# Kernel tuning notes

Hardware: AMD Instinct MI355X
Metric: run time of the kernel (lower is better)

Reference implementation:

```python
import jax, jax.numpy as jnp
import numpy as np

D_DIM = 1024
K_DIM = 16
B, L = 4, 2048

def setup_inputs() -> dict:
    key = jax.random.key(0)
    kx, ky, kz, kw, kb = jax.random.split(key, 5)
    x = jax.random.normal(kx, (B, L, D_DIM), dtype=jnp.float32)
    y = jax.random.normal(ky, (B, L, D_DIM), dtype=jnp.float32)
    z = jax.random.normal(kz, (B, L, D_DIM), dtype=jnp.float32)
    bound = 1.0 / np.sqrt(3 * D_DIM)  # torch Linear init scale
    W = jax.random.uniform(kw, (K_DIM * D_DIM, 3 * D_DIM), dtype=jnp.float32, minval=-bound, maxval=bound)
    b = jax.random.uniform(kb, (K_DIM * D_DIM,), dtype=jnp.float32, minval=-bound, maxval=bound)
    return {"x": x, "y": y, "z": z, "W": W, "b": b}

def reference(x, y, z, W, b):
    Bsz, Lsz, D = x.shape
    inp = jnp.concatenate([x, y, z], axis=-1)                 # (B, L, 3D)
    kernel = jnp.einsum('blc,fc->blf', inp, W) + b            # (B, L, k*D)
    kernel = kernel.reshape(Bsz, Lsz, D, K_DIM)               # (B, L, D, k)
    # einsum 'bldk,bld->bld' == sum over k, then elementwise multiply
    return kernel.sum(axis=-1) * (x * y)
```

## Files before the change

kernel.cpp:

```cpp
#include <hip/hip_runtime.h>

#define M_ROWS 8192
#define N_DIM  1024
#define K3     3072
#define KD     16
#define NKT    48
#define BM     256
#define BN     128
#define BK     64
#define LDS_A  (BM * BK)
#define LDS_B  (BN * BK)
#define LDS_TILE (LDS_A + LDS_B)

typedef __bf16 bf16x8 __attribute__((ext_vector_type(8)));
typedef float  f32x4  __attribute__((ext_vector_type(4)));

__device__ __forceinline__ unsigned short f2bf(float f) {
  return __builtin_bit_cast(unsigned short, (__bf16)f);
}
__device__ __forceinline__ float bf2f(unsigned short u) {
  return __builtin_bit_cast(float, (unsigned int)u << 16);
}
__device__ __forceinline__ ushort4 pack4(f32x4 f) {
  ushort4 o; o.x = f2bf(f.x); o.y = f2bf(f.y); o.z = f2bf(f.z); o.w = f2bf(f.w);
  return o;
}
__device__ __forceinline__ f32x4 ntld4(const f32x4* p) {
  return __builtin_nontemporal_load(p);
}

__device__ __forceinline__ void async16(const void* g, void* l) {
  __builtin_amdgcn_global_load_lds(
      (const __attribute__((address_space(1))) unsigned int*)g,
      (__attribute__((address_space(3))) unsigned int*)l, 16, 0, 0);
}

__global__ __launch_bounds__(256) void wsum_kernel(
    const f32x4* __restrict__ W4, const float* __restrict__ b,
    ushort4* __restrict__ Wsum4, float* __restrict__ bsum)
{
  int bid = blockIdx.x;
  int tid = threadIdx.x;
  if (bid < 3072) {
    int g  = bid * 256 + tid;
    int d  = g / 768;
    int cq = g - d * 768;
    const f32x4* wrow = W4 + (size_t)d * (KD * K3 / 4);
    f32x4 s = ntld4(&wrow[cq]);
    #pragma unroll
    for (int k = 1; k < KD; ++k)
      s += ntld4(&wrow[(size_t)k * (K3 / 4) + cq]);
    Wsum4[g] = pack4(s);
  } else {
    int d = (bid - 3072) * 256 + tid;
    if (d < N_DIM) {
      float s = 0.f;
      #pragma unroll
      for (int k = 0; k < KD; ++k) s += b[d * KD + k];
      bsum[d] = s;
    }
  }
}

__global__ __launch_bounds__(256) void convert_kernel(
    const f32x4* __restrict__ x, const f32x4* __restrict__ y, const f32x4* __restrict__ z,
    ushort4* __restrict__ Ib4, ushort4* __restrict__ P4)
{
  int bid = blockIdx.x;
  int tid = threadIdx.x;
  int i = bid * 256 + tid;
  f32x4 fx = ntld4(&x[i]), fy = ntld4(&y[i]), fz = ntld4(&z[i]);
  size_t rb = (size_t)bid * 768;
  Ib4[rb + tid]       = pack4(fx);
  Ib4[rb + 256 + tid] = pack4(fy);
  Ib4[rb + 512 + tid] = pack4(fz);
  P4[i] = pack4(fx * fy);
}

__global__ __launch_bounds__(512, 2) void gemm_ep_kernel(
    const unsigned short* __restrict__ Ib, const unsigned short* __restrict__ Wsum,
    const float* __restrict__ bsum, const unsigned short* __restrict__ P,
    float* __restrict__ out)
{
  extern __shared__ unsigned short lds[];

  int bid = blockIdx.x;
  int swz = (bid & 7) * 32 + (bid >> 3);
  int mt = swz >> 3;
  int nt = swz & 7;
  int m0 = mt * BM, n0 = nt * BN;

  int tid  = threadIdx.x;
  int lane = tid & 63;
  int wid  = tid >> 6;
  int wr = wid >> 1, wc = wid & 1;
  int fr = lane & 15;
  int hi = lane >> 4;

  int row0 = tid >> 3;
  int ch0  = tid & 7;
  int dofs = tid * 16;
  int sc   = (ch0 ^ (row0 & 7)) << 3;

  const unsigned short* Abase = Ib   + (size_t)m0 * K3;
  const unsigned short* Bbase = Wsum + (size_t)n0 * K3;

  f32x4 acc[4][4];
  #pragma unroll
  for (int i = 0; i < 4; ++i)
    #pragma unroll
    for (int j = 0; j < 4; ++j)
      acc[i][j] = f32x4{0.f, 0.f, 0.f, 0.f};

  auto STAGE = [&](int slot, int t) {
    char* dst = (char*)(lds + slot * LDS_TILE);
    int k0 = t << 6;
    #pragma unroll
    for (int r = 0; r < 4; ++r)
      async16(Abase + (size_t)(row0 + r * 64) * K3 + k0 + sc, dst + dofs + r * 8192);
    char* dstB = dst + 2 * LDS_A;
    #pragma unroll
    for (int r = 0; r < 2; ++r)
      async16(Bbase + (size_t)(row0 + r * 64) * K3 + k0 + sc, dstB + dofs + r * 8192);
  };

  auto LOAD8 = [&](const unsigned short* pA, int kk, bf16x8 (&a)[4], bf16x8 (&b)[4]) {
    const unsigned short* pB = pA + LDS_A;
    int c = (kk << 2) + hi;
    #pragma unroll
    for (int i = 0; i < 4; ++i) {
      int R = wr * 64 + i * 16 + fr;
      a[i] = *(const bf16x8*)&pA[(R << 6) + ((c ^ (R & 7)) << 3)];
    }
    #pragma unroll
    for (int j = 0; j < 4; ++j) {
      int R = wc * 64 + j * 16 + fr;
      b[j] = *(const bf16x8*)&pB[(R << 6) + ((c ^ (R & 7)) << 3)];
    }
  };
  auto MFMA16 = [&](bf16x8 (&a)[4], bf16x8 (&b)[4]) {
    __builtin_amdgcn_s_setprio(1);
    #pragma unroll
    for (int i = 0; i < 4; ++i)
      #pragma unroll
      for (int j = 0; j < 4; ++j)
        acc[i][j] = __builtin_amdgcn_mfma_f32_16x16x32_bf16(a[i], b[j], acc[i][j], 0, 0, 0);
    __builtin_amdgcn_s_setprio(0);
  };

  bf16x8 aA[4], bA[4], aB[4], bB[4];

  auto TILE = [&](int t, const unsigned short* pCur, const unsigned short* pNext,
                  int stSlot) {
    bool st = (t + 2) < NKT;
    LOAD8(pCur, 1, aB, bB);
    __builtin_amdgcn_sched_barrier(0);
    if (st) STAGE(stSlot, t + 2);
    asm volatile("s_waitcnt lgkmcnt(8)" ::: "memory");
    __builtin_amdgcn_sched_barrier(0);
    MFMA16(aA, bA);
    if (st) asm volatile("s_waitcnt vmcnt(6)" ::: "memory");
    else    asm volatile("s_waitcnt vmcnt(0)" ::: "memory");
    __builtin_amdgcn_s_barrier();
    LOAD8(pNext, 0, aA, bA);
    __builtin_amdgcn_sched_barrier(0);
    asm volatile("s_waitcnt lgkmcnt(8)" ::: "memory");
    __builtin_amdgcn_sched_barrier(0);
    MFMA16(aB, bB);
    __builtin_amdgcn_s_barrier();
  };

  const unsigned short* s0 = lds;
  const unsigned short* s1 = lds + LDS_TILE;
  const unsigned short* s2 = lds + 2 * LDS_TILE;

  STAGE(0, 0);
  STAGE(1, 1);
  asm volatile("s_waitcnt vmcnt(6)" ::: "memory");
  __builtin_amdgcn_s_barrier();
  LOAD8(s0, 0, aA, bA);
  __builtin_amdgcn_sched_barrier(0);

  #pragma unroll 1
  for (int t = 0; t < NKT; t += 3) {
    TILE(t,     s0, s1, 2);
    TILE(t + 1, s1, s2, 0);
    TILE(t + 2, s2, s0, 1);
  }

  #pragma unroll
  for (int i = 0; i < 4; ++i) {
    #pragma unroll
    for (int j = 0; j < 4; ++j) {
      int n = n0 + wc * 64 + j * 16 + fr;
      float bs = bsum[n];
      #pragma unroll
      for (int r = 0; r < 4; ++r) {
        int m = m0 + wr * 64 + i * 16 + hi * 4 + r;
        size_t idx = (size_t)m * N_DIM + n;
        unsigned short pv = __builtin_nontemporal_load(&P[idx]);
        __builtin_nontemporal_store((acc[i][j][r] + bs) * bf2f(pv), &out[idx]);
      }
    }
  }
}

extern "C" void kernel_launch(void* const* d_in, const int* in_sizes, int n_in,
                              void* d_out, int out_size, void* d_ws, size_t ws_size,
                              hipStream_t stream) {
  const float* x = (const float*)d_in[0];
  const float* y = (const float*)d_in[1];
  const float* z = (const float*)d_in[2];
  const float* W = (const float*)d_in[3];
  const float* b = (const float*)d_in[4];
  float* out = (float*)d_out;

  unsigned short* Ib   = (unsigned short*)d_ws;
  unsigned short* Wsum = Ib + (size_t)M_ROWS * K3;
  unsigned short* P    = Wsum + (size_t)N_DIM * K3;
  float*          bsum = (float*)(P + (size_t)M_ROWS * N_DIM);

  wsum_kernel<<<3076, 256, 0, stream>>>((const f32x4*)W, b, (ushort4*)Wsum, bsum);

  convert_kernel<<<8192, 256, 0, stream>>>(
      (const f32x4*)x, (const f32x4*)y, (const f32x4*)z,
      (ushort4*)Ib, (ushort4*)P);

  gemm_ep_kernel<<<256, 512, 3 * LDS_TILE * sizeof(unsigned short), stream>>>(
      Ib, Wsum, bsum, P, out);
}
```

Measured before the change: 126.8 us.

## Shrink GEMM tile to 128x128 with 256 threads and double-buffered LDS

The M tile of the GEMM is halved to 128 and the block size to 256 threads, which doubles the grid to 512 blocks so they fill more of the CUs. The triple-buffered, cross-tile software pipeline becomes a simpler double buffer: each K tile loads both LDS fragments, stages the next tile, runs the MFMAs, then waits and synchronises. This is meant to improve occupancy and CU coverage. In exchange, operand reuse per block drops, so more global traffic is needed for the B operand, and the wait for global loads now sits at the end of every K tile, which exposes more latency.

```diff
diff --git a/kernel.cpp b/kernel.cpp
--- a/kernel.cpp
+++ b/kernel.cpp
@@ -5,12 +5,11 @@
 #define K3     3072
 #define KD     16
 #define NKT    48
-#define BM     256
+#define BM     128
 #define BN     128
 #define BK     64
 #define LDS_A  (BM * BK)
-#define LDS_B  (BN * BK)
-#define LDS_TILE (LDS_A + LDS_B)
+#define LDS_TILE (2 * LDS_A)
 
 typedef __bf16 bf16x8 __attribute__((ext_vector_type(8)));
 typedef float  f32x4  __attribute__((ext_vector_type(4)));
@@ -77,15 +76,15 @@
   P4[i] = pack4(fx * fy);
 }
 
-__global__ __launch_bounds__(512, 2) void gemm_ep_kernel(
+__global__ __launch_bounds__(256, 2) void gemm_ep_kernel(
     const unsigned short* __restrict__ Ib, const unsigned short* __restrict__ Wsum,
     const float* __restrict__ bsum, const unsigned short* __restrict__ P,
     float* __restrict__ out)
 {
-  extern __shared__ unsigned short lds[];
+  __shared__ unsigned short lds[2 * LDS_TILE];
 
   int bid = blockIdx.x;
-  int swz = (bid & 7) * 32 + (bid >> 3);
+  int swz = (bid & 7) * 64 + (bid >> 3);
   int mt = swz >> 3;
   int nt = swz & 7;
   int m0 = mt * BM, n0 = nt * BN;
@@ -113,18 +112,19 @@
       acc[i][j] = f32x4{0.f, 0.f, 0.f, 0.f};
 
   auto STAGE = [&](int slot, int t) {
-    char* dst = (char*)(lds + slot * LDS_TILE);
+    char* dstA = (char*)(lds + slot * LDS_TILE);
+    char* dstB = dstA + 2 * LDS_A;
     int k0 = t << 6;
     #pragma unroll
     for (int r = 0; r < 4; ++r)
-      async16(Abase + (size_t)(row0 + r * 64) * K3 + k0 + sc, dst + dofs + r * 8192);
-    char* dstB = dst + 2 * LDS_A;
-    #pragma unroll
-    for (int r = 0; r < 2; ++r)
-      async16(Bbase + (size_t)(row0 + r * 64) * K3 + k0 + sc, dstB + dofs + r * 8192);
-  };
-
-  auto LOAD8 = [&](const unsigned short* pA, int kk, bf16x8 (&a)[4], bf16x8 (&b)[4]) {
+      async16(Abase + (size_t)(row0 + r * 32) * K3 + k0 + sc, dstA + dofs + r * 4096);
+    #pragma unroll
+    for (int r = 0; r < 4; ++r)
+      async16(Bbase + (size_t)(row0 + r * 32) * K3 + k0 + sc, dstB + dofs + r * 4096);
+  };
+
+  auto LOAD8 = [&](int slot, int kk, bf16x8 (&a)[4], bf16x8 (&b)[4]) {
+    const unsigned short* pA = lds + slot * LDS_TILE;
     const unsigned short* pB = pA + LDS_A;
     int c = (kk << 2) + hi;
     #pragma unroll
@@ -150,42 +150,30 @@
 
   bf16x8 aA[4], bA[4], aB[4], bB[4];
 
-  auto TILE = [&](int t, const unsigned short* pCur, const unsigned short* pNext,
-                  int stSlot) {
-    bool st = (t + 2) < NKT;
-    LOAD8(pCur, 1, aB, bB);
-    __builtin_amdgcn_sched_barrier(0);
-    if (st) STAGE(stSlot, t + 2);
+  auto TILE = [&](int t, int slot, bool st) {
+    LOAD8(slot, 0, aA, bA);
+    __builtin_amdgcn_sched_barrier(0);
+    LOAD8(slot, 1, aB, bB);
+    __builtin_amdgcn_sched_barrier(0);
+    if (st) STAGE(slot ^ 1, t + 1);
     asm volatile("s_waitcnt lgkmcnt(8)" ::: "memory");
     __builtin_amdgcn_sched_barrier(0);
     MFMA16(aA, bA);
-    if (st) asm volatile("s_waitcnt vmcnt(6)" ::: "memory");
-    else    asm volatile("s_waitcnt vmcnt(0)" ::: "memory");
+    asm volatile("s_waitcnt lgkmcnt(0)" ::: "memory");
+    __builtin_amdgcn_sched_barrier(0);
+    MFMA16(aB, bB);
+    asm volatile("s_waitcnt vmcnt(0)" ::: "memory");
     __builtin_amdgcn_s_barrier();
-    LOAD8(pNext, 0, aA, bA);
-    __builtin_amdgcn_sched_barrier(0);
-    asm volatile("s_waitcnt lgkmcnt(8)" ::: "memory");
-    __builtin_amdgcn_sched_barrier(0);
-    MFMA16(aB, bB);
-    __builtin_amdgcn_s_barrier();
-  };
-
-  const unsigned short* s0 = lds;
-  const unsigned short* s1 = lds + LDS_TILE;
-  const unsigned short* s2 = lds + 2 * LDS_TILE;
+  };
 
   STAGE(0, 0);
-  STAGE(1, 1);
-  asm volatile("s_waitcnt vmcnt(6)" ::: "memory");
+  asm volatile("s_waitcnt vmcnt(0)" ::: "memory");
   __builtin_amdgcn_s_barrier();
-  LOAD8(s0, 0, aA, bA);
-  __builtin_amdgcn_sched_barrier(0);
 
   #pragma unroll 1
-  for (int t = 0; t < NKT; t += 3) {
-    TILE(t,     s0, s1, 2);
-    TILE(t + 1, s1, s2, 0);
-    TILE(t + 2, s2, s0, 1);
+  for (int t = 0; t < NKT; t += 2) {
+    TILE(t,     0, true);
+    TILE(t + 1, 1, t + 2 < NKT);
   }
 
   #pragma unroll
@@ -226,6 +214,5 @@
       (const f32x4*)x, (const f32x4*)y, (const f32x4*)z,
       (ushort4*)Ib, (ushort4*)P);
 
-  gemm_ep_kernel<<<256, 512, 3 * LDS_TILE * sizeof(unsigned short), stream>>>(
-      Ib, Wsum, bsum, P, out);
-}
+  gemm_ep_kernel<<<512, 256, 0, stream>>>(Ib, Wsum, bsum, P, out);
+}
```

After: 125.8 us. No clear change (-0.8%).
